# Performance work log

Measured on AMD Instinct MI355X. Metric: run time of the kernel, lower is better.

The kernel has to match this reference:

```python
import math
import jax, jax.numpy as jnp
import numpy as np
from jax import lax

# Block_mamba(dim=192): x = x + Mamba(LN1(x)); x = x + EinFFT(LN2(x), H, W)
DIM = 192
D_STATE = 64
D_CONV = 4
EXPAND = 2
D_INNER = EXPAND * DIM          # 384
DT_RANK = math.ceil(DIM / 16)   # 12
NUM_BLOCKS = 4                  # EinFFT hardcoded
BLOCK_SIZE = DIM // NUM_BLOCKS  # 48
LAMBDA = 0.01                   # softshrink threshold


def setup_inputs() -> dict:
    key = jax.random.key(0)
    ks = jax.random.split(key, 20)
    B, N, C = 4, 1024, DIM
    s = 0.02
    x = jax.random.normal(ks[0], (B, N, C), jnp.float32)
    inp = {
        "x": x,
        "ln1_w": jnp.ones((C,), jnp.float32),
        "ln1_b": jnp.zeros((C,), jnp.float32),
        "in_proj_w": jax.random.normal(ks[1], (2 * D_INNER, C), jnp.float32) * s,
        "conv_w": jax.random.normal(ks[2], (D_INNER, 1, D_CONV), jnp.float32) * 0.1,
        "conv_b": jnp.zeros((D_INNER,), jnp.float32),
        "x_proj_w": jax.random.normal(ks[3], (DT_RANK + 2 * D_STATE, D_INNER), jnp.float32) * s,
        "dt_proj_w": jax.random.normal(ks[4], (D_INNER, DT_RANK), jnp.float32) * (DT_RANK ** -0.5),
        "dt_proj_b": jax.random.uniform(ks[5], (D_INNER,), jnp.float32, -4.0, -2.0),
        "A_log": jnp.log(jnp.broadcast_to(jnp.arange(1, D_STATE + 1, dtype=jnp.float32), (D_INNER, D_STATE))),
        "D": jnp.ones((D_INNER,), jnp.float32),
        "out_proj_w": jax.random.normal(ks[6], (C, D_INNER), jnp.float32) * s,
        "ln2_w": jnp.ones((C,), jnp.float32),
        "ln2_b": jnp.zeros((C,), jnp.float32),
        "cw1": jax.random.normal(ks[7], (2, NUM_BLOCKS, BLOCK_SIZE, BLOCK_SIZE), jnp.float32) * s,
        "cw2": jax.random.normal(ks[8], (2, NUM_BLOCKS, BLOCK_SIZE, BLOCK_SIZE), jnp.float32) * s,
        "cb1": jax.random.normal(ks[9], (2, NUM_BLOCKS, BLOCK_SIZE), jnp.float32) * s,
        "cb2": jax.random.normal(ks[10], (2, NUM_BLOCKS, BLOCK_SIZE), jnp.float32) * s,
        "H": 32,
        "W": 32,
    }
    return inp


def layer_norm(x, w, b, eps=1e-5):
    mu = jnp.mean(x, axis=-1, keepdims=True)
    var = jnp.var(x, axis=-1, keepdims=True)
    return (x - mu) * lax.rsqrt(var + eps) * w + b


def mamba(x, in_proj_w, conv_w, conv_b, x_proj_w, dt_proj_w, dt_proj_b, A_log, D):
    B, L, C = x.shape
    xz = jnp.einsum('blc,ec->ble', x, in_proj_w)          # [B,L,2*D_INNER]
    xm, z = jnp.split(xz, 2, axis=-1)                      # each [B,L,D_INNER]
    # causal depthwise conv1d (torch pads both sides then slices [:, :, :L])
    xc = lax.conv_general_dilated(
        xm.transpose(0, 2, 1), conv_w, (1,), [(D_CONV - 1, 0)],
        dimension_numbers=('NCH', 'OIH', 'NCH'), feature_group_count=D_INNER)
    xm = jax.nn.silu(xc + conv_b[None, :, None]).transpose(0, 2, 1)  # [B,L,D_INNER]
    dbc = jnp.einsum('bld,ed->ble', xm, x_proj_w)
    dt, Bm, Cm = jnp.split(dbc, [DT_RANK, DT_RANK + D_STATE], axis=-1)
    delta = jax.nn.softplus(jnp.einsum('blr,dr->bld', dt, dt_proj_w) + dt_proj_b)  # [B,L,D_INNER]
    A = -jnp.exp(A_log)                                    # [D_INNER, D_STATE]

    def step(h, inp):
        d_t, B_t, C_t, x_t = inp                           # [B,d],[B,n],[B,n],[B,d]
        dA = jnp.exp(d_t[:, :, None] * A)                  # [B,d,n]
        h = h * dA + (d_t * x_t)[:, :, None] * B_t[:, None, :]
        y = jnp.einsum('bdn,bn->bd', h, C_t)
        return h, y

    h0 = jnp.zeros((B, D_INNER, D_STATE), x.dtype)
    xs = (delta.transpose(1, 0, 2), Bm.transpose(1, 0, 2), Cm.transpose(1, 0, 2), xm.transpose(1, 0, 2))
    _, ys = lax.scan(step, h0, xs)                         # ys: [L,B,d]
    y = ys.transpose(1, 0, 2) + xm * D
    y = y * jax.nn.silu(z)
    return jnp.einsum('bld,cd->blc', y, out_proj_w_global[0])


# small trick to keep mamba signature tidy
out_proj_w_global = [None]


def einfft(x, cw1, cw2, cb1, cb2):
    B, N, C = x.shape
    xv = x.reshape(B, N, NUM_BLOCKS, BLOCK_SIZE)
    pad1 = (1 << math.ceil(math.log2(N))) - N
    pad2 = (1 << math.ceil(math.log2(NUM_BLOCKS))) - NUM_BLOCKS
    if pad1 or pad2:
        xv = jnp.pad(xv, ((0, 0), (0, pad1), (0, pad2), (0, 0)))
    X = jnp.fft.fft2(xv, axes=(1, 2), norm='ortho')
    mul = lambda t, w: jnp.einsum('Bnbd,bdk->Bnbk', t, w)
    r1 = jax.nn.relu(mul(X.real, cw1[0]) - mul(X.imag, cw1[1]) + cb1[0])
    i1 = jax.nn.relu(mul(X.real, cw1[1]) + mul(X.imag, cw1[0]) + cb1[1])
    r2 = mul(r1, cw2[0]) - mul(i1, cw2[1]) + cb2[0]
    i2 = mul(r1, cw2[1]) + mul(i1, cw2[0]) + cb2[1]
    ss = lambda v: jnp.where(v > LAMBDA, v - LAMBDA, jnp.where(v < -LAMBDA, v + LAMBDA, jnp.zeros((), v.dtype)))
    Z = ss(r2) + 1j * ss(i2)
    y = jnp.fft.ifft2(Z, axes=(1, 2), norm='ortho')[:, :N, :NUM_BLOCKS, :]
    return y.real.reshape(B, N, C)  # torch .to(real dtype) keeps real part


def reference(x, ln1_w, ln1_b, in_proj_w, conv_w, conv_b, x_proj_w, dt_proj_w, dt_proj_b,
              A_log, D, out_proj_w, ln2_w, ln2_b, cw1, cw2, cb1, cb2, H, W):
    out_proj_w_global[0] = out_proj_w
    x = x + mamba(layer_norm(x, ln1_w, ln1_b), in_proj_w, conv_w, conv_b,
                  x_proj_w, dt_proj_w, dt_proj_b, A_log, D)
    x = x + einfft(layer_norm(x, ln2_w, ln2_b), cw1, cw2, cb1, cb2)
    return x
```

## Files before the change

### kernel.cpp

```cpp
#include <hip/hip_runtime.h>
#include <math.h>

#define PI_F 3.14159265358979323846f

__device__ __forceinline__ float lane_bcast(float v, int l) {
  return __int_as_float(__builtin_amdgcn_readlane(__float_as_int(v), l));
}

__device__ __forceinline__ float wave_reduce_sum(float v) {
  v += __shfl_xor(v, 32, 64);
  v += __shfl_xor(v, 16, 64);
  v += __shfl_xor(v, 8, 64);
  v += __shfl_xor(v, 4, 64);
  v += __shfl_xor(v, 2, 64);
  v += __shfl_xor(v, 1, 64);
  return v;
}

__global__ __launch_bounds__(256) void ln_kernel(const float* __restrict__ x,
    const float* __restrict__ w, const float* __restrict__ b, float* __restrict__ o) {
  int row = blockIdx.x * 4 + (threadIdx.x >> 6);
  int lane = threadIdx.x & 63;
  const float* xr = x + (size_t)row * 192;
  float v0 = xr[lane], v1 = xr[lane + 64], v2 = xr[lane + 128];
  float s  = wave_reduce_sum(v0 + v1 + v2);
  float s2 = wave_reduce_sum(v0 * v0 + v1 * v1 + v2 * v2);
  float mu  = s * (1.f / 192.f);
  float var = s2 * (1.f / 192.f) - mu * mu;
  float rs  = rsqrtf(var + 1e-5f);
  float* orow = o + (size_t)row * 192;
  orow[lane]       = (v0 - mu) * rs * w[lane]       + b[lane];
  orow[lane + 64]  = (v1 - mu) * rs * w[lane + 64]  + b[lane + 64];
  orow[lane + 128] = (v2 - mu) * rs * w[lane + 128] + b[lane + 128];
}

__global__ __launch_bounds__(256) void ln2t_kernel(const float* __restrict__ x,
    const float* __restrict__ w, const float* __restrict__ b, float* __restrict__ xT) {
  __shared__ float xt[32][193];
  __shared__ float mu_s[32], rs_s[32];
  int blk = blockIdx.x;
  int Bi = blk >> 5;
  int t0 = (blk & 31) * 32;
  int tid = threadIdx.x;
  const float* xb = x + ((size_t)(Bi * 1024 + t0)) * 192;
  for (int i = tid; i < 32 * 192; i += 256) {
    xt[i / 192][i % 192] = xb[i];
  }
  __syncthreads();
  int row = tid >> 3, seg = tid & 7;
  float s = 0.f, s2 = 0.f;
  const float* xr = &xt[row][seg * 24];
#pragma unroll
  for (int k = 0; k < 24; ++k) { float v = xr[k]; s += v; s2 += v * v; }
  s  += __shfl_xor(s, 1, 64);  s  += __shfl_xor(s, 2, 64);  s  += __shfl_xor(s, 4, 64);
  s2 += __shfl_xor(s2, 1, 64); s2 += __shfl_xor(s2, 2, 64); s2 += __shfl_xor(s2, 4, 64);
  if (seg == 0) {
    float mu = s * (1.f / 192.f);
    float var = s2 * (1.f / 192.f) - mu * mu;
    mu_s[row] = mu;
    rs_s[row] = rsqrtf(var + 1e-5f);
  }
  __syncthreads();
  for (int i = tid; i < 32 * 192; i += 256) {
    int ch = i >> 5, r2 = i & 31;
    float v = (xt[r2][ch] - mu_s[r2]) * rs_s[r2] * w[ch] + b[ch];
    xT[((size_t)(Bi * 192 + ch)) * 1024 + t0 + r2] = v;
  }
}

__global__ __launch_bounds__(256) void gemm_tn(const float* __restrict__ A,
    const float* __restrict__ W, const float* __restrict__ res, float* __restrict__ C,
    int M, int N, int K) {
  __shared__ float As[2][32][68];
  __shared__ float Ws[2][32][68];
  int tid = threadIdx.x;
  int m0 = blockIdx.y * 64, n0 = blockIdx.x * 64;
  int tr = tid >> 4, tc = tid & 15;
  int sm  = tid >> 3;
  int skq = tid & 7;
  float4 aP[2], wP[2];
#pragma unroll
  for (int j = 0; j < 2; ++j) {
    int m = sm + j * 32;
    aP[j] = *(const float4*)(A + (size_t)(m0 + m) * K + skq * 4);
    int n = n0 + m;
    if (n < N) wP[j] = *(const float4*)(W + (size_t)n * K + skq * 4);
    else       wP[j] = make_float4(0.f, 0.f, 0.f, 0.f);
  }
#pragma unroll
  for (int j = 0; j < 2; ++j) {
    int m = sm + j * 32;
    As[0][skq * 4 + 0][m] = aP[j].x;
    As[0][skq * 4 + 1][m] = aP[j].y;
    As[0][skq * 4 + 2][m] = aP[j].z;
    As[0][skq * 4 + 3][m] = aP[j].w;
    Ws[0][skq * 4 + 0][m] = wP[j].x;
    Ws[0][skq * 4 + 1][m] = wP[j].y;
    Ws[0][skq * 4 + 2][m] = wP[j].z;
    Ws[0][skq * 4 + 3][m] = wP[j].w;
  }
  __syncthreads();
  float acc[4][4] = {{0.f}};
  int nk = K >> 5;
  for (int it = 0; it < nk; ++it) {
    int cur = it & 1, nxt = cur ^ 1;
    if (it + 1 < nk) {
      int kk = (it + 1) << 5;
#pragma unroll
      for (int j = 0; j < 2; ++j) {
        int m = sm + j * 32;
        aP[j] = *(const float4*)(A + (size_t)(m0 + m) * K + kk + skq * 4);
        int n = n0 + m;
        if (n < N) wP[j] = *(const float4*)(W + (size_t)n * K + kk + skq * 4);
        else       wP[j] = make_float4(0.f, 0.f, 0.f, 0.f);
      }
    }
#pragma unroll
    for (int k = 0; k < 32; ++k) {
      float4 a4 = *(const float4*)&As[cur][k][tr * 4];
      float4 w4 = *(const float4*)&Ws[cur][k][tc * 4];
      float a[4] = {a4.x, a4.y, a4.z, a4.w};
      float bb[4] = {w4.x, w4.y, w4.z, w4.w};
#pragma unroll
      for (int i = 0; i < 4; ++i)
#pragma unroll
        for (int j = 0; j < 4; ++j)
          acc[i][j] = fmaf(a[i], bb[j], acc[i][j]);
    }
    if (it + 1 < nk) {
#pragma unroll
      for (int j = 0; j < 2; ++j) {
        int m = sm + j * 32;
        As[nxt][skq * 4 + 0][m] = aP[j].x;
        As[nxt][skq * 4 + 1][m] = aP[j].y;
        As[nxt][skq * 4 + 2][m] = aP[j].z;
        As[nxt][skq * 4 + 3][m] = aP[j].w;
        Ws[nxt][skq * 4 + 0][m] = wP[j].x;
        Ws[nxt][skq * 4 + 1][m] = wP[j].y;
        Ws[nxt][skq * 4 + 2][m] = wP[j].z;
        Ws[nxt][skq * 4 + 3][m] = wP[j].w;
      }
      __syncthreads();
    }
  }
#pragma unroll
  for (int i = 0; i < 4; ++i) {
    int m = m0 + tr * 4 + i;
#pragma unroll
    for (int j = 0; j < 4; ++j) {
      int n = n0 + tc * 4 + j;
      if (n < N) {
        float v = acc[i][j];
        if (res) v += res[m * N + n];
        C[m * N + n] = v;
      }
    }
  }
}

__global__ __launch_bounds__(256) void gemm_tn32(const float* __restrict__ A,
    const float* __restrict__ W, const float* __restrict__ res, float* __restrict__ C,
    int M, int N, int K) {
  __shared__ float As[2][32][36];
  __shared__ float Ws[2][32][68];
  int tid = threadIdx.x;
  int m0 = blockIdx.y * 32, n0 = blockIdx.x * 64;
  int tr = tid >> 4, tc = tid & 15;
  int sm  = tid >> 3;
  int skq = tid & 7;
  float4 aP, wP[2];
  aP = *(const float4*)(A + (size_t)(m0 + sm) * K + skq * 4);
#pragma unroll
  for (int j = 0; j < 2; ++j) {
    int n = n0 + sm + j * 32;
    if (n < N) wP[j] = *(const float4*)(W + (size_t)n * K + skq * 4);
    else       wP[j] = make_float4(0.f, 0.f, 0.f, 0.f);
  }
  As[0][skq * 4 + 0][sm] = aP.x;
  As[0][skq * 4 + 1][sm] = aP.y;
  As[0][skq * 4 + 2][sm] = aP.z;
  As[0][skq * 4 + 3][sm] = aP.w;
#pragma unroll
  for (int j = 0; j < 2; ++j) {
    int n = sm + j * 32;
    Ws[0][skq * 4 + 0][n] = wP[j].x;
    Ws[0][skq * 4 + 1][n] = wP[j].y;
    Ws[0][skq * 4 + 2][n] = wP[j].z;
    Ws[0][skq * 4 + 3][n] = wP[j].w;
  }
  __syncthreads();
  float acc[2][4] = {{0.f}};
  int nk = K >> 5;
  for (int it = 0; it < nk; ++it) {
    int cur = it & 1, nxt = cur ^ 1;
    if (it + 1 < nk) {
      int kk = (it + 1) << 5;
      aP = *(const float4*)(A + (size_t)(m0 + sm) * K + kk + skq * 4);
#pragma unroll
      for (int j = 0; j < 2; ++j) {
        int n = n0 + sm + j * 32;
        if (n < N) wP[j] = *(const float4*)(W + (size_t)n * K + kk + skq * 4);
        else       wP[j] = make_float4(0.f, 0.f, 0.f, 0.f);
      }
    }
#pragma unroll
    for (int k = 0; k < 32; ++k) {
      float2 a2 = *(const float2*)&As[cur][k][tr * 2];
      float4 w4 = *(const float4*)&Ws[cur][k][tc * 4];
      float a[2] = {a2.x, a2.y};
      float bb[4] = {w4.x, w4.y, w4.z, w4.w};
#pragma unroll
      for (int i = 0; i < 2; ++i)
#pragma unroll
        for (int j = 0; j < 4; ++j)
          acc[i][j] = fmaf(a[i], bb[j], acc[i][j]);
    }
    if (it + 1 < nk) {
      As[nxt][skq * 4 + 0][sm] = aP.x;
      As[nxt][skq * 4 + 1][sm] = aP.y;
      As[nxt][skq * 4 + 2][sm] = aP.z;
      As[nxt][skq * 4 + 3][sm] = aP.w;
#pragma unroll
      for (int j = 0; j < 2; ++j) {
        int n = sm + j * 32;
        Ws[nxt][skq * 4 + 0][n] = wP[j].x;
        Ws[nxt][skq * 4 + 1][n] = wP[j].y;
        Ws[nxt][skq * 4 + 2][n] = wP[j].z;
        Ws[nxt][skq * 4 + 3][n] = wP[j].w;
      }
      __syncthreads();
    }
  }
#pragma unroll
  for (int i = 0; i < 2; ++i) {
    int m = m0 + tr * 2 + i;
#pragma unroll
    for (int j = 0; j < 4; ++j) {
      int n = n0 + tc * 4 + j;
      if (n < N) {
        float v = acc[i][j];
        if (res) v += res[m * N + n];
        C[m * N + n] = v;
      }
    }
  }
}

__global__ __launch_bounds__(256) void gemm_at32(const float* __restrict__ AT,
    const float* __restrict__ W, const float* __restrict__ res, float* __restrict__ C,
    int M, int N, int K) {
  __shared__ float As[2][32][36];
  __shared__ float Ws[2][32][68];
  int tid = threadIdx.x;
  int m0 = blockIdx.y * 32, n0 = blockIdx.x * 64;
  int bb = m0 >> 10;
  int t0 = m0 & 1023;
  const float* Ab = AT + ((size_t)bb * K) * 1024 + t0;
  int tr = tid >> 4, tc = tid & 15;
  int sm  = tid >> 3;
  int skq = tid & 7;
  float4 aP, wP[2];
  aP = *(const float4*)(Ab + (size_t)sm * 1024 + skq * 4);
#pragma unroll
  for (int j = 0; j < 2; ++j) {
    int n = n0 + sm + j * 32;
    if (n < N) wP[j] = *(const float4*)(W + (size_t)n * K + skq * 4);
    else       wP[j] = make_float4(0.f, 0.f, 0.f, 0.f);
  }
  *(float4*)&As[0][sm][skq * 4] = aP;
#pragma unroll
  for (int j = 0; j < 2; ++j) {
    int n = sm + j * 32;
    Ws[0][skq * 4 + 0][n] = wP[j].x;
    Ws[0][skq * 4 + 1][n] = wP[j].y;
    Ws[0][skq * 4 + 2][n] = wP[j].z;
    Ws[0][skq * 4 + 3][n] = wP[j].w;
  }
  __syncthreads();
  float acc[2][4] = {{0.f}};
  int nk = K >> 5;
  for (int it = 0; it < nk; ++it) {
    int cur = it & 1, nxt = cur ^ 1;
    if (it + 1 < nk) {
      int kk = (it + 1) << 5;
      aP = *(const float4*)(Ab + (size_t)(kk + sm) * 1024 + skq * 4);
#pragma unroll
      for (int j = 0; j < 2; ++j) {
        int n = n0 + sm + j * 32;
        if (n < N) wP[j] = *(const float4*)(W + (size_t)n * K + kk + skq * 4);
        else       wP[j] = make_float4(0.f, 0.f, 0.f, 0.f);
      }
    }
#pragma unroll
    for (int k = 0; k < 32; ++k) {
      float2 a2 = *(const float2*)&As[cur][k][tr * 2];
      float4 w4 = *(const float4*)&Ws[cur][k][tc * 4];
      float a[2] = {a2.x, a2.y};
      float bb4[4] = {w4.x, w4.y, w4.z, w4.w};
#pragma unroll
      for (int i = 0; i < 2; ++i)
#pragma unroll
        for (int j = 0; j < 4; ++j)
          acc[i][j] = fmaf(a[i], bb4[j], acc[i][j]);
    }
    if (it + 1 < nk) {
      *(float4*)&As[nxt][sm][skq * 4] = aP;
#pragma unroll
      for (int j = 0; j < 2; ++j) {
        int n = sm + j * 32;
        Ws[nxt][skq * 4 + 0][n] = wP[j].x;
        Ws[nxt][skq * 4 + 1][n] = wP[j].y;
        Ws[nxt][skq * 4 + 2][n] = wP[j].z;
        Ws[nxt][skq * 4 + 3][n] = wP[j].w;
      }
      __syncthreads();
    }
  }
#pragma unroll
  for (int i = 0; i < 2; ++i) {
    int m = m0 + tr * 2 + i;
#pragma unroll
    for (int j = 0; j < 4; ++j) {
      int n = n0 + tc * 4 + j;
      if (n < N) {
        float v = acc[i][j];
        if (res) v += res[m * N + n];
        C[m * N + n] = v;
      }
    }
  }
}

__global__ __launch_bounds__(256) void conv_silu(const float* __restrict__ xz,
    const float* __restrict__ cw, const float* __restrict__ cb, float* __restrict__ xc) {
  int e4 = blockIdx.x * 256 + threadIdx.x;
  if (e4 >= 4 * 1024 * 96) return;
  int d4 = e4 % 96;
  int t  = (e4 / 96) % 1024;
  int b  = e4 / (96 * 1024);
  int d = d4 * 4;
  const float* base = xz + (size_t)(b * 1024) * 768 + d;
  float4 acc = *(const float4*)(cb + d);
  const float4* cwv = (const float4*)(cw + d * 4);
  float4 c0 = cwv[0], c1 = cwv[1], c2 = cwv[2], c3 = cwv[3];
#pragma unroll
  for (int j = 0; j < 4; ++j) {
    int tt = t - 3 + j;
    if (tt >= 0) {
      float4 v = *(const float4*)(base + (size_t)tt * 768);
      float w0 = (&c0.x)[j], w1 = (&c1.x)[j], w2 = (&c2.x)[j], w3 = (&c3.x)[j];
      acc.x = fmaf(v.x, w0, acc.x);
      acc.y = fmaf(v.y, w1, acc.y);
      acc.z = fmaf(v.z, w2, acc.z);
      acc.w = fmaf(v.w, w3, acc.w);
    }
  }
  float4 o;
  o.x = acc.x / (1.f + __expf(-acc.x));
  o.y = acc.y / (1.f + __expf(-acc.y));
  o.z = acc.z / (1.f + __expf(-acc.z));
  o.w = acc.w / (1.f + __expf(-acc.w));
  *(float4*)(xc + ((size_t)(b * 1024 + t) * 384) + d) = o;
}

__global__ __launch_bounds__(256) void delta_trans(const float* __restrict__ dbc,
    const float* __restrict__ dtw, const float* __restrict__ dtb,
    const float* __restrict__ xc, float* __restrict__ dltT, float* __restrict__ duT) {
  __shared__ float dts[64][13];
  __shared__ float xt[64][65];
  int blk = blockIdx.x;
  int b  = blk / 96;
  int rem = blk % 96;
  int tt = rem / 6, dd = rem % 6;
  int t0 = tt * 64, d0 = dd * 64;
  int tid = threadIdx.x;
  for (int i = tid; i < 64 * 12; i += 256) {
    int tl = i / 12, r = i % 12;
    dts[tl][r] = dbc[((size_t)b * 1024 + t0 + tl) * 140 + r];
  }
  {
    int col = tid & 63, rg = tid >> 6;
#pragma unroll
    for (int j = 0; j < 16; ++j) {
      int row = j * 4 + rg;
      xt[row][col] = xc[((size_t)b * 1024 + t0 + row) * 384 + d0 + col];
    }
  }
  __syncthreads();
  int tl = tid & 63, grp = tid >> 6;
#pragma unroll
  for (int j = 0; j < 16; ++j) {
    int dl = grp * 16 + j;
    int d = d0 + dl;
    float s = dtb[d];
#pragma unroll
    for (int r = 0; r < 12; ++r) s += dts[tl][r] * dtw[d * 12 + r];
    float dlt = (s > 20.f) ? s : log1pf(__expf(s));
    size_t ob = ((size_t)b * 384 + d) * 1024 + t0 + tl;
    dltT[ob] = dlt;
    duT[ob]  = dlt * xt[tl][dl];
  }
}

__global__ __launch_bounds__(64) void scan_single(const float* __restrict__ dltT,
    const float* __restrict__ duT, const float* __restrict__ dbc,
    const float* __restrict__ A_log, const float* __restrict__ xc,
    const float* __restrict__ xz, const float* __restrict__ Dvec,
    float* __restrict__ yT) {
  __shared__ float tile[16][65];
  int bd = blockIdx.x;
  int b = bd / 384, d = bd % 384;
  int lane = threadIdx.x;
  float A = -__expf(A_log[d * 64 + lane]) * 1.44269504f;
  const float* dT = dltT + ((size_t)b * 384 + d) * 1024;
  const float* uT = duT  + ((size_t)b * 384 + d) * 1024;
  const float* Bp = dbc + ((size_t)b * 1024) * 140 + 12 + lane;
  const float* Cp = Bp + 64;
  float ddv = Dvec[d];
  float* yp = yT + ((size_t)b * 384 + d) * 1024;
  const float* xcp = xc + ((size_t)b * 1024) * 384 + d;
  const float* xzp = xz + ((size_t)b * 1024) * 768 + 384 + d;
  int tq = lane & 15;
  int q  = lane >> 4;
  float h = 0.f;
  for (int seg = 0; seg < 16; ++seg) {
    float dv64 = dT[seg * 64 + lane];
    float du64 = uT[seg * 64 + lane];
    for (int tb = 0; tb < 64; tb += 16) {
      int ts = seg * 64 + tb;
      float Bv[16], Cv[16];
#pragma unroll
      for (int i = 0; i < 16; ++i) {
        size_t ro = (size_t)(ts + i) * 140;
        Bv[i] = Bp[ro];
        Cv[i] = Cp[ro];
      }
      float xcv = 0.f, zv = 0.f;
      if (lane < 16) {
        xcv = xcp[(size_t)(ts + lane) * 384];
        zv  = xzp[(size_t)(ts + lane) * 768];
      }
#pragma unroll
      for (int i = 0; i < 16; ++i) {
        float sdv = lane_bcast(dv64, tb + i);
        float sdu = lane_bcast(du64, tb + i);
        float a = exp2f(sdv * A);
        h = fmaf(h, a, sdu * Bv[i]);
        tile[i][lane] = h * Cv[i];
      }
      const float* trow = &tile[tq][q * 16];
      float s = 0.f;
#pragma unroll
      for (int i = 0; i < 16; ++i) s += trow[i];
      s += __shfl_xor(s, 16, 64);
      s += __shfl_xor(s, 32, 64);
      if (lane < 16) {
        float sg = zv / (1.f + __expf(-zv));
        yp[ts + lane] = (s + xcv * ddv) * sg;
      }
    }
  }
}

__device__ __forceinline__ int rev4_10(int i) {
  unsigned r = __brev((unsigned)i) >> 22;
  return (int)(((r & 0x155u) << 1) | ((r >> 1) & 0x155u));
}

__device__ __forceinline__ void fft1024r4(float* __restrict__ re,
    float* __restrict__ im, const float* __restrict__ twc,
    const float* __restrict__ tws, int tid, float sgn) {
  for (int i = tid; i < 1024; i += 256) {
    int r = rev4_10(i);
    if (i < r) {
      float t = re[i]; re[i] = re[r]; re[r] = t;
      t = im[i]; im[i] = im[r]; im[r] = t;
    }
  }
  __syncthreads();
  {
    float4 ar = *(float4*)&re[tid * 4];
    float4 ai = *(float4*)&im[tid * 4];
    float apc_r = ar.x + ar.z, amc_r = ar.x - ar.z;
    float apc_i = ai.x + ai.z, amc_i = ai.x - ai.z;
    float bpd_r = ar.y + ar.w, bmd_r = ar.y - ar.w;
    float bpd_i = ai.y + ai.w, bmd_i = ai.y - ai.w;
    float4 yr, yi;
    yr.x = apc_r + bpd_r;        yi.x = apc_i + bpd_i;
    yr.z = apc_r - bpd_r;        yi.z = apc_i - bpd_i;
    yr.y = amc_r - sgn * bmd_i;  yi.y = amc_i + sgn * bmd_r;
    yr.w = amc_r + sgn * bmd_i;  yi.w = amc_i - sgn * bmd_r;
    *(float4*)&re[tid * 4] = yr;
    *(float4*)&im[tid * 4] = yi;
  }
  __syncthreads();
#pragma unroll
  for (int s = 1; s < 5; ++s) {
    int L = 1 << (2 * s);
    int tstep = 256 >> (2 * s);
    int j = tid & (L - 1);
    int base = ((tid >> (2 * s)) << (2 * s + 2)) + j;
    int i0 = base, i1 = base + L, i2 = base + 2 * L, i3 = base + 3 * L;
    int x1i = j * tstep;
    float w1c = twc[x1i],     w1s = tws[x1i];
    float w2c = twc[2 * x1i], w2s = tws[2 * x1i];
    float w3c = twc[3 * x1i], w3s = tws[3 * x1i];
    float ar_ = re[i0], ai_ = im[i0];
    float br_ = re[i1], bi_ = im[i1];
    float cr_ = re[i2], ci_ = im[i2];
    float dr_ = re[i3], di_ = im[i3];
    float tbr = br_ * w1c - bi_ * w1s, tbi = br_ * w1s + bi_ * w1c;
    float tcr = cr_ * w2c - ci_ * w2s, tci = cr_ * w2s + ci_ * w2c;
    float tdr = dr_ * w3c - di_ * w3s, tdi = dr_ * w3s + di_ * w3c;
    float apc_r = ar_ + tcr, amc_r = ar_ - tcr;
    float apc_i = ai_ + tci, amc_i = ai_ - tci;
    float bpd_r = tbr + tdr, bmd_r = tbr - tdr;
    float bpd_i = tbi + tdi, bmd_i = tbi - tdi;
    re[i0] = apc_r + bpd_r;       im[i0] = apc_i + bpd_i;
    re[i2] = apc_r - bpd_r;       im[i2] = apc_i - bpd_i;
    re[i1] = amc_r - sgn * bmd_i; im[i1] = amc_i + sgn * bmd_r;
    re[i3] = amc_r + sgn * bmd_i; im[i3] = amc_i - sgn * bmd_r;
    __syncthreads();
  }
}

__global__ __launch_bounds__(256) void fft_fwd(const float* __restrict__ x2T,
    float* __restrict__ Xre, float* __restrict__ Xim) {
  __shared__ float re[1024];
  __shared__ float im[1024];
  __shared__ float twc[768];
  __shared__ float tws[768];
  int blk = blockIdx.x;
  int c = blk & 3;
  int rest = blk >> 2;
  int d = rest % 48, Bi = rest / 48;
  int tid = threadIdx.x;
  for (int k = tid; k < 768; k += 256) {
    float sv, cv;
    __sincosf(-PI_F * (float)k * (1.f / 512.f), &sv, &cv);
    twc[k] = cv; tws[k] = sv;
  }
  const float* pb = x2T + ((size_t)(Bi * 192 + d)) * 1024;
  for (int n = tid; n < 1024; n += 256) {
    float v0 = pb[n];
    float v1 = pb[48 * 1024 + n];
    float v2 = pb[96 * 1024 + n];
    float v3 = pb[144 * 1024 + n];
    float rr, ii;
    if (c == 0)      { rr = v0 + v1 + v2 + v3; ii = 0.f; }
    else if (c == 1) { rr = v0 - v2;           ii = -(v1 - v3); }
    else if (c == 2) { rr = v0 - v1 + v2 - v3; ii = 0.f; }
    else             { rr = v0 - v2;           ii = (v1 - v3); }
    re[n] = rr; im[n] = ii;
  }
  __syncthreads();
  fft1024r4(re, im, twc, tws, tid, -1.0f);
  float* xo_r = Xre + ((size_t)((Bi * 4 + c) * 48 + d)) * 1024;
  float* xo_i = Xim + ((size_t)((Bi * 4 + c) * 48 + d)) * 1024;
  for (int k = tid; k < 1024; k += 256) {
    xo_r[k] = re[k] * (1.f / 64.f);
    xo_i[k] = im[k] * (1.f / 64.f);
  }
}

__global__ __launch_bounds__(256) void mix_fused(float* __restrict__ Xre,
    float* __restrict__ Xim, const float* __restrict__ cw1,
    const float* __restrict__ cw2, const float* __restrict__ cb1,
    const float* __restrict__ cb2) {
  __shared__ float r1s[4][48][4];
  __shared__ float i1s[4][48][4];
  int w = threadIdx.x >> 6;
  int j = threadIdx.x & 63;
  int rg = blockIdx.x * 4 + w;
  int kq = rg & 255;
  int b  = (rg >> 8) & 3;
  int Bi = rg >> 10;
  int k0 = kq * 4;
  size_t xbase = ((size_t)((Bi * 4 + b) * 48)) * 1024 + k0;
  if (j < 48) {
    const float* wr = cw1 + b * 2304;
    const float* wi = cw1 + 9216 + b * 2304;
    float b1r = cb1[b * 48 + j], b1i = cb1[192 + b * 48 + j];
    float ar[4] = {b1r, b1r, b1r, b1r};
    float ai[4] = {b1i, b1i, b1i, b1i};
#pragma unroll 8
    for (int dd = 0; dd < 48; ++dd) {
      float4 xr = *(const float4*)(Xre + xbase + (size_t)dd * 1024);
      float4 xi = *(const float4*)(Xim + xbase + (size_t)dd * 1024);
      float wrv = wr[dd * 48 + j], wiv = wi[dd * 48 + j];
      ar[0] = fmaf(xr.x, wrv, ar[0]); ar[0] = fmaf(-xi.x, wiv, ar[0]);
      ai[0] = fmaf(xr.x, wiv, ai[0]); ai[0] = fmaf(xi.x, wrv, ai[0]);
      ar[1] = fmaf(xr.y, wrv, ar[1]); ar[1] = fmaf(-xi.y, wiv, ar[1]);
      ai[1] = fmaf(xr.y, wiv, ai[1]); ai[1] = fmaf(xi.y, wrv, ai[1]);
      ar[2] = fmaf(xr.z, wrv, ar[2]); ar[2] = fmaf(-xi.z, wiv, ar[2]);
      ai[2] = fmaf(xr.z, wiv, ai[2]); ai[2] = fmaf(xi.z, wrv, ai[2]);
      ar[3] = fmaf(xr.w, wrv, ar[3]); ar[3] = fmaf(-xi.w, wiv, ar[3]);
      ai[3] = fmaf(xr.w, wiv, ai[3]); ai[3] = fmaf(xi.w, wrv, ai[3]);
    }
    float4 r1v, i1v;
    r1v.x = fmaxf(ar[0], 0.f); r1v.y = fmaxf(ar[1], 0.f);
    r1v.z = fmaxf(ar[2], 0.f); r1v.w = fmaxf(ar[3], 0.f);
    i1v.x = fmaxf(ai[0], 0.f); i1v.y = fmaxf(ai[1], 0.f);
    i1v.z = fmaxf(ai[2], 0.f); i1v.w = fmaxf(ai[3], 0.f);
    *(float4*)&r1s[w][j][0] = r1v;
    *(float4*)&i1s[w][j][0] = i1v;
    const float* wr2 = cw2 + b * 2304;
    const float* wi2 = cw2 + 9216 + b * 2304;
    float b2r = cb2[b * 48 + j], b2i = cb2[192 + b * 48 + j];
    float a2r[4] = {b2r, b2r, b2r, b2r};
    float a2i[4] = {b2i, b2i, b2i, b2i};
#pragma unroll 8
    for (int dd = 0; dd < 48; ++dd) {
      float4 rv = *(const float4*)&r1s[w][dd][0];
      float4 iv = *(const float4*)&i1s[w][dd][0];
      float wrv = wr2[dd * 48 + j], wiv = wi2[dd * 48 + j];
      a2r[0] = fmaf(rv.x, wrv, a2r[0]); a2r[0] = fmaf(-iv.x, wiv, a2r[0]);
      a2i[0] = fmaf(rv.x, wiv, a2i[0]); a2i[0] = fmaf(iv.x, wrv, a2i[0]);
      a2r[1] = fmaf(rv.y, wrv, a2r[1]); a2r[1] = fmaf(-iv.y, wiv, a2r[1]);
      a2i[1] = fmaf(rv.y, wiv, a2i[1]); a2i[1] = fmaf(iv.y, wrv, a2i[1]);
      a2r[2] = fmaf(rv.z, wrv, a2r[2]); a2r[2] = fmaf(-iv.z, wiv, a2r[2]);
      a2i[2] = fmaf(rv.z, wiv, a2i[2]); a2i[2] = fmaf(iv.z, wrv, a2i[2]);
      a2r[3] = fmaf(rv.w, wrv, a2r[3]); a2r[3] = fmaf(-iv.w, wiv, a2r[3]);
      a2i[3] = fmaf(rv.w, wiv, a2i[3]); a2i[3] = fmaf(iv.w, wrv, a2i[3]);
    }
    float4 zr, zi;
#pragma unroll
    for (int r = 0; r < 4; ++r) {
      float vr = a2r[r], vi = a2i[r];
      (&zr.x)[r] = (vr > 0.01f) ? vr - 0.01f : ((vr < -0.01f) ? vr + 0.01f : 0.f);
      (&zi.x)[r] = (vi > 0.01f) ? vi - 0.01f : ((vi < -0.01f) ? vi + 0.01f : 0.f);
    }
    size_t obase = ((size_t)((Bi * 4 + b) * 48 + j)) * 1024 + k0;
    *(float4*)(Xre + obase) = zr;
    *(float4*)(Xim + obase) = zi;
  }
}

__global__ __launch_bounds__(256) void fft_inv(const float* __restrict__ Zre,
    const float* __restrict__ Zim, const float* __restrict__ x1, float* __restrict__ out) {
  __shared__ float re[1024];
  __shared__ float im[1024];
  __shared__ float twc[768];
  __shared__ float tws[768];
  int blk = blockIdx.x;
  int c = blk & 3;
  int rest = blk >> 2;
  int d = rest % 48, Bi = rest / 48;
  int tid = threadIdx.x;
  for (int k = tid; k < 768; k += 256) {
    float sv, cv;
    __sincosf(PI_F * (float)k * (1.f / 512.f), &sv, &cv);
    twc[k] = cv; tws[k] = sv;
  }
  const float* zr0 = Zre + ((size_t)((Bi * 4) * 48 + d)) * 1024;
  const float* zi0 = Zim + ((size_t)((Bi * 4) * 48 + d)) * 1024;
  const int cs = 48 * 1024;
  for (int k = tid; k < 1024; k += 256) {
    float r0 = zr0[k], r1v = zr0[cs + k], r2 = zr0[2 * cs + k], r3 = zr0[3 * cs + k];
    float i0 = zi0[k], i1v = zi0[cs + k], i2 = zi0[2 * cs + k], i3 = zi0[3 * cs + k];
    float rr, ii;
    if (c == 0)      { rr = r0 + r1v + r2 + r3;  ii = i0 + i1v + i2 + i3; }
    else if (c == 1) { rr = r0 - i1v - r2 + i3;  ii = i0 + r1v - i2 - r3; }
    else if (c == 2) { rr = r0 - r1v + r2 - r3;  ii = i0 - i1v + i2 - i3; }
    else             { rr = r0 + i1v - r2 - i3;  ii = i0 - r1v - i2 + r3; }
    re[k] = rr; im[k] = ii;
  }
  __syncthreads();
  fft1024r4(re, im, twc, tws, tid, 1.0f);
  for (int n = tid; n < 1024; n += 256) {
    size_t o = (size_t)(Bi * 1024 + n) * 192 + c * 48 + d;
    out[o] = x1[o] + re[n] * (1.f / 64.f);
  }
}

extern "C" void kernel_launch(void* const* d_in, const int* in_sizes, int n_in,
                              void* d_out, int out_size, void* d_ws, size_t ws_size,
                              hipStream_t stream) {
  const float* x         = (const float*)d_in[0];
  const float* ln1_w     = (const float*)d_in[1];
  const float* ln1_b     = (const float*)d_in[2];
  const float* in_proj_w = (const float*)d_in[3];
  const float* conv_w    = (const float*)d_in[4];
  const float* conv_b    = (const float*)d_in[5];
  const float* x_proj_w  = (const float*)d_in[6];
  const float* dt_proj_w = (const float*)d_in[7];
  const float* dt_proj_b = (const float*)d_in[8];
  const float* A_log     = (const float*)d_in[9];
  const float* Dvec      = (const float*)d_in[10];
  const float* out_proj_w= (const float*)d_in[11];
  const float* ln2_w     = (const float*)d_in[12];
  const float* ln2_b     = (const float*)d_in[13];
  const float* cw1       = (const float*)d_in[14];
  const float* cw2       = (const float*)d_in[15];
  const float* cb1       = (const float*)d_in[16];
  const float* cb2       = (const float*)d_in[17];
  float* out = (float*)d_out;
  float* ws  = (float*)d_ws;

  float* xz   = ws;
  float* xc   = xz  + 3145728;
  float* dbc  = xc  + 1572864;
  float* dltT = dbc + 573440;
  float* yvT  = dltT + 1572864;
  float* xln  = yvT + 1572864;
  float* x2T  = xln + 786432;
  float* Xre  = x2T + 786432;
  float* Xim  = Xre + 786432;
  float* duT = Xre;
  float* x1 = xln;

  ln_kernel<<<1024, 256, 0, stream>>>(x, ln1_w, ln1_b, xln);
  gemm_tn<<<dim3(12, 64), 256, 0, stream>>>(xln, in_proj_w, nullptr, xz, 4096, 768, 192);
  conv_silu<<<1536, 256, 0, stream>>>(xz, conv_w, conv_b, xc);
  gemm_tn32<<<dim3(3, 128), 256, 0, stream>>>(xc, x_proj_w, nullptr, dbc, 4096, 140, 384);
  delta_trans<<<384, 256, 0, stream>>>(dbc, dt_proj_w, dt_proj_b, xc, dltT, duT);
  scan_single<<<1536, 64, 0, stream>>>(dltT, duT, dbc, A_log, xc, xz, Dvec, yvT);
  gemm_at32<<<dim3(3, 128), 256, 0, stream>>>(yvT, out_proj_w, x, x1, 4096, 192, 384);
  ln2t_kernel<<<128, 256, 0, stream>>>(x1, ln2_w, ln2_b, x2T);
  fft_fwd<<<768, 256, 0, stream>>>(x2T, Xre, Xim);
  mix_fused<<<1024, 256, 0, stream>>>(Xre, Xim, cw1, cw2, cb1, cb2);
  fft_inv<<<768, 256, 0, stream>>>(Xre, Xim, x1, out);
}
```

Baseline: 342.4 us.

## Software-pipeline scan loads with double-buffered B/C/xc/z register sets

Restructures the selective-scan loop to prefetch the next 16-step group's B, C, xc and z values, plus the next segment's delta and du, into a second register bank while the current group computes. The aim is to hide global memory latency behind the serial recurrence in the one-wave-per-block scan kernel. The launch bound is changed to (64,1) to allow more registers. This raises register pressure and may reduce occupancy.

```diff
diff --git a/kernel.cpp b/kernel.cpp
--- a/kernel.cpp
+++ b/kernel.cpp
@@ -402,7 +402,47 @@
   }
 }
 
-__global__ __launch_bounds__(64) void scan_single(const float* __restrict__ dltT,
+#define SCAN_GBODY(G, BC, CC, XCV, ZVV, BN, CN, XCN, ZVN)                  \
+  {                                                                        \
+    int ts_ = (G) * 16;                                                    \
+    if ((G) + 1 < 64) {                                                    \
+      int tn_ = ts_ + 16;                                                  \
+      _Pragma("unroll")                                                    \
+      for (int i = 0; i < 16; ++i) {                                       \
+        size_t ro = (size_t)(tn_ + i) * 140;                               \
+        BN[i] = Bp[ro]; CN[i] = Cp[ro];                                    \
+      }                                                                    \
+      if (lane < 16) { XCN = xcp[(size_t)(tn_ + lane) * 384];              \
+                       ZVN = xzp[(size_t)(tn_ + lane) * 768]; }            \
+      if (((G) & 3) == 2) {                                                \
+        int sn_ = ((G) >> 2) + 1;                                          \
+        if (sn_ < 16) { dvN = dT[sn_ * 64 + lane];                         \
+                        duN = uT[sn_ * 64 + lane]; }                       \
+      }                                                                    \
+    }                                                                      \
+    int tb_ = ts_ & 63;                                                    \
+    _Pragma("unroll")                                                      \
+    for (int i = 0; i < 16; ++i) {                                         \
+      float sdv = lane_bcast(dvC, tb_ + i);                                \
+      float sdu = lane_bcast(duC, tb_ + i);                                \
+      float a = exp2f(sdv * A);                                            \
+      h = fmaf(h, a, sdu * BC[i]);                                         \
+      tile[i][lane] = h * CC[i];                                           \
+    }                                                                      \
+    const float* trow_ = &tile[tq][q * 16];                                \
+    float s_ = 0.f;                                                        \
+    _Pragma("unroll")                                                      \
+    for (int i = 0; i < 16; ++i) s_ += trow_[i];                           \
+    s_ += __shfl_xor(s_, 16, 64);                                          \
+    s_ += __shfl_xor(s_, 32, 64);                                          \
+    if (lane < 16) {                                                       \
+      float sg_ = ZVV / (1.f + __expf(-ZVV));                              \
+      yp[ts_ + lane] = (s_ + XCV * ddv) * sg_;                             \
+    }                                                                      \
+    if (((G) & 3) == 3) { dvC = dvN; duC = duN; }                          \
+  }
+
+__global__ __launch_bounds__(64, 1) void scan_single(const float* __restrict__ dltT,
     const float* __restrict__ duT, const float* __restrict__ dbc,
     const float* __restrict__ A_log, const float* __restrict__ xc,
     const float* __restrict__ xz, const float* __restrict__ Dvec,
@@ -423,42 +463,28 @@
   int tq = lane & 15;
   int q  = lane >> 4;
   float h = 0.f;
-  for (int seg = 0; seg < 16; ++seg) {
-    float dv64 = dT[seg * 64 + lane];
-    float du64 = uT[seg * 64 + lane];
-    for (int tb = 0; tb < 64; tb += 16) {
-      int ts = seg * 64 + tb;
-      float Bv[16], Cv[16];
-#pragma unroll
-      for (int i = 0; i < 16; ++i) {
-        size_t ro = (size_t)(ts + i) * 140;
-        Bv[i] = Bp[ro];
-        Cv[i] = Cp[ro];
-      }
-      float xcv = 0.f, zv = 0.f;
-      if (lane < 16) {
-        xcv = xcp[(size_t)(ts + lane) * 384];
-        zv  = xzp[(size_t)(ts + lane) * 768];
-      }
-#pragma unroll
-      for (int i = 0; i < 16; ++i) {
-        float sdv = lane_bcast(dv64, tb + i);
-        float sdu = lane_bcast(du64, tb + i);
-        float a = exp2f(sdv * A);
-        h = fmaf(h, a, sdu * Bv[i]);
-        tile[i][lane] = h * Cv[i];
-      }
-      const float* trow = &tile[tq][q * 16];
-      float s = 0.f;
-#pragma unroll
-      for (int i = 0; i < 16; ++i) s += trow[i];
-      s += __shfl_xor(s, 16, 64);
-      s += __shfl_xor(s, 32, 64);
-      if (lane < 16) {
-        float sg = zv / (1.f + __expf(-zv));
-        yp[ts + lane] = (s + xcv * ddv) * sg;
-      }
-    }
+
+  float Ba[16], Ca[16], Bb[16], Cb[16];
+  float dvC, duC, dvN = 0.f, duN = 0.f;
+  float xcA = 0.f, zvA = 0.f, xcB = 0.f, zvB = 0.f;
+
+  dvC = dT[lane];
+  duC = uT[lane];
+#pragma unroll
+  for (int i = 0; i < 16; ++i) {
+    size_t ro = (size_t)i * 140;
+    Ba[i] = Bp[ro];
+    Ca[i] = Cp[ro];
+  }
+  if (lane < 16) {
+    xcA = xcp[(size_t)lane * 384];
+    zvA = xzp[(size_t)lane * 768];
+  }
+
+  for (int gp = 0; gp < 32; ++gp) {
+    int g0 = gp * 2;
+    SCAN_GBODY(g0,     Ba, Ca, xcA, zvA, Bb, Cb, xcB, zvB)
+    SCAN_GBODY(g0 + 1, Bb, Cb, xcB, zvB, Ba, Ca, xcA, zvA)
   }
 }
 
```

After: 338.8 us. About the same (-1.1%).

## Split selective scan into producer and consumer waves with double-buffered LDS

Applied to the files above, without the earlier changes.

The scan kernel now runs two wavefronts per block: one wave prefetches the next 16-step chunk of B, C, delta, du, xc and z into double-buffered shared memory while the other performs the recurrence on the current chunk. This hides global-load latency from the serial scan dependency chain. The cost is a block-wide barrier every 16 steps, more shared memory per block, and an idle wave's worth of occupancy.

```diff
diff --git a/kernel.cpp b/kernel.cpp
--- a/kernel.cpp
+++ b/kernel.cpp
@@ -402,44 +402,87 @@
   }
 }
 
-__global__ __launch_bounds__(64) void scan_single(const float* __restrict__ dltT,
+__global__ __launch_bounds__(128) void scan_pc(const float* __restrict__ dltT,
     const float* __restrict__ duT, const float* __restrict__ dbc,
     const float* __restrict__ A_log, const float* __restrict__ xc,
     const float* __restrict__ xz, const float* __restrict__ Dvec,
     float* __restrict__ yT) {
+  __shared__ float Bs[2][16][64];
+  __shared__ float Cs[2][16][64];
+  __shared__ float dvs[2][64], dus[2][64];
+  __shared__ float xcs[2][16], zvs[2][16];
   __shared__ float tile[16][65];
   int bd = blockIdx.x;
   int b = bd / 384, d = bd % 384;
-  int lane = threadIdx.x;
-  float A = -__expf(A_log[d * 64 + lane]) * 1.44269504f;
+  int tid = threadIdx.x;
+  int wv = tid >> 6;
+  int lane = tid & 63;
   const float* dT = dltT + ((size_t)b * 384 + d) * 1024;
   const float* uT = duT  + ((size_t)b * 384 + d) * 1024;
-  const float* Bp = dbc + ((size_t)b * 1024) * 140 + 12 + lane;
-  const float* Cp = Bp + 64;
-  float ddv = Dvec[d];
+  const float* Bbase = dbc + (size_t)(b * 1024) * 140 + 12;
+  const float* xcp = xc + (size_t)(b * 1024) * 384 + d;
+  const float* xzp = xz + (size_t)(b * 1024) * 768 + 384 + d;
   float* yp = yT + ((size_t)b * 384 + d) * 1024;
-  const float* xcp = xc + ((size_t)b * 1024) * 384 + d;
-  const float* xzp = xz + ((size_t)b * 1024) * 768 + 384 + d;
-  int tq = lane & 15;
-  int q  = lane >> 4;
-  float h = 0.f;
-  for (int seg = 0; seg < 16; ++seg) {
-    float dv64 = dT[seg * 64 + lane];
-    float du64 = uT[seg * 64 + lane];
-    for (int tb = 0; tb < 64; tb += 16) {
-      int ts = seg * 64 + tb;
+
+  float A = 0.f, ddv = 0.f;
+  int tq = lane & 15, q = lane >> 4;
+  if (wv == 1) {
+#pragma unroll
+    for (int i = 0; i < 16; ++i) {
+      size_t ro = (size_t)i * 140 + lane;
+      Bs[0][i][lane] = Bbase[ro];
+      Cs[0][i][lane] = Bbase[ro + 64];
+    }
+    dvs[0][lane] = dT[lane];
+    dus[0][lane] = uT[lane];
+    if (lane < 16) {
+      xcs[0][lane] = xcp[(size_t)lane * 384];
+      zvs[0][lane] = xzp[(size_t)lane * 768];
+    }
+  } else {
+    A = -__expf(A_log[d * 64 + lane]) * 1.44269504f;
+    ddv = Dvec[d];
+  }
+  __syncthreads();
+
+  float h = 0.f, dv64 = 0.f, du64 = 0.f;
+  for (int g = 0; g < 64; ++g) {
+    int cur = g & 1, nxt = cur ^ 1;
+    if (wv == 1) {
+      if (g < 63) {
+        int ts1 = (g + 1) * 16;
+#pragma unroll
+        for (int i = 0; i < 16; ++i) {
+          size_t ro = (size_t)(ts1 + i) * 140 + lane;
+          Bs[nxt][i][lane] = Bbase[ro];
+          Cs[nxt][i][lane] = Bbase[ro + 64];
+        }
+        if (lane < 16) {
+          xcs[nxt][lane] = xcp[(size_t)(ts1 + lane) * 384];
+          zvs[nxt][lane] = xzp[(size_t)(ts1 + lane) * 768];
+        }
+        if (((g + 1) & 3) == 0) {
+          int sseg = (g + 1) >> 2;
+          int sl = sseg & 1;
+          dvs[sl][lane] = dT[sseg * 64 + lane];
+          dus[sl][lane] = uT[sseg * 64 + lane];
+        }
+      }
+    } else {
+      if ((g & 3) == 0) {
+        int sl = (g >> 2) & 1;
+        dv64 = dvs[sl][lane];
+        du64 = dus[sl][lane];
+      }
+      int ts = g * 16, tb = ts & 63;
       float Bv[16], Cv[16];
 #pragma unroll
       for (int i = 0; i < 16; ++i) {
-        size_t ro = (size_t)(ts + i) * 140;
-        Bv[i] = Bp[ro];
-        Cv[i] = Cp[ro];
+        Bv[i] = Bs[cur][i][lane];
+        Cv[i] = Cs[cur][i][lane];
       }
       float xcv = 0.f, zv = 0.f;
-      if (lane < 16) {
-        xcv = xcp[(size_t)(ts + lane) * 384];
-        zv  = xzp[(size_t)(ts + lane) * 768];
-      }
+      if (lane < 16) { xcv = xcs[cur][lane]; zv = zvs[cur][lane]; }
 #pragma unroll
       for (int i = 0; i < 16; ++i) {
         float sdv = lane_bcast(dv64, tb + i);
@@ -449,16 +492,17 @@
         tile[i][lane] = h * Cv[i];
       }
       const float* trow = &tile[tq][q * 16];
-      float s = 0.f;
-#pragma unroll
-      for (int i = 0; i < 16; ++i) s += trow[i];
-      s += __shfl_xor(s, 16, 64);
-      s += __shfl_xor(s, 32, 64);
+      float s_ = 0.f;
+#pragma unroll
+      for (int i = 0; i < 16; ++i) s_ += trow[i];
+      s_ += __shfl_xor(s_, 16, 64);
+      s_ += __shfl_xor(s_, 32, 64);
       if (lane < 16) {
         float sg = zv / (1.f + __expf(-zv));
-        yp[ts + lane] = (s + xcv * ddv) * sg;
-      }
-    }
+        yp[ts + lane] = (s_ + xcv * ddv) * sg;
+      }
+    }
+    __syncthreads();
   }
 }
 
@@ -714,7 +758,7 @@
   conv_silu<<<1536, 256, 0, stream>>>(xz, conv_w, conv_b, xc);
   gemm_tn32<<<dim3(3, 128), 256, 0, stream>>>(xc, x_proj_w, nullptr, dbc, 4096, 140, 384);
   delta_trans<<<384, 256, 0, stream>>>(dbc, dt_proj_w, dt_proj_b, xc, dltT, duT);
-  scan_single<<<1536, 64, 0, stream>>>(dltT, duT, dbc, A_log, xc, xz, Dvec, yvT);
+  scan_pc<<<1536, 128, 0, stream>>>(dltT, duT, dbc, A_log, xc, xz, Dvec, yvT);
   gemm_at32<<<dim3(3, 128), 256, 0, stream>>>(yvT, out_proj_w, x, x1, 4096, 192, 384);
   ln2t_kernel<<<128, 256, 0, stream>>>(x1, ln2_w, ln2_b, x2T);
   fft_fwd<<<768, 256, 0, stream>>>(x2T, Xre, Xim);
```

New measurement: 350.5 us. 1.02x slower.
